# Optimization experiments

Hardware: AMD Instinct MI355X
Metric: run time of the kernel (lower is better)

Reference implementation:

```python
import jax, jax.numpy as jnp
import numpy as np

N_PARTIAL = 1024  # matches init_kwargs


def setup_inputs() -> dict:
    key = jax.random.key(0)
    k1, k2 = jax.random.split(key)
    B, H, L = 8, 768, 4096
    x = jax.random.normal(k1, (B, H, L), dtype=jnp.float32)
    k = jax.random.normal(k2, (H, L), dtype=jnp.float32)
    return {"x": x, "k": k}


def reference(x, k):
    # FFT-based causal long convolution with low-pass frequency truncation.
    L = x.shape[-1]
    N = 2 * L  # zero-pad to 2L for linear (non-circular) convolution
    x_dtype = x.dtype
    x_f = jnp.fft.rfft(x.astype(jnp.float32), n=N)          # [B, H, N//2+1] complex64
    k_f = jnp.fft.rfft(k.astype(jnp.float32), n=N)          # [H, N//2+1]   complex64
    # zero out all frequency bins >= N_partial // 2 (low-pass truncation of the kernel)
    freqs = jnp.arange(N // 2 + 1)
    k_f = jnp.where(freqs < N_PARTIAL // 2, k_f, jnp.zeros((), dtype=k_f.dtype))
    y_f = x_f * k_f                                          # broadcast over batch
    y = jnp.fft.irfft(y_f, n=N)[..., :L].astype(x_dtype)     # [B, H, L]
    return y
```

## Files before the change

kernel.cpp:

```cpp
#include <hip/hip_runtime.h>
#include <math.h>

#define LSEQ 4096
#define NFFT 8192
#define NF   512
#define NF2  1024
#define NH   768
#define NBH  6144
#define MROWS 6912

typedef __attribute__((ext_vector_type(8))) short short8;
typedef __attribute__((ext_vector_type(4))) float floatx4;

__device__ __forceinline__ unsigned short f2bf(float f) {
    unsigned int u = __float_as_uint(f);
    u += 0x7fff + ((u >> 16) & 1);
    return (unsigned short)(u >> 16);
}

__global__ void build_T1(unsigned short* __restrict__ T1) {
    int idx = blockIdx.x * blockDim.x + threadIdx.x;
    int f2 = idx >> 12;
    int n = idx & (LSEQ - 1);
    int f = f2 >> 1;
    int p = (f * n) & (NFFT - 1);
    float th = (float)p * (float)(2.0 * M_PI / (double)NFFT);
    float s, c;
    sincosf(th, &s, &c);
    T1[idx] = f2bf((f2 & 1) ? s : c);
}

__global__ void build_T2(unsigned short* __restrict__ T2) {
    int idx = blockIdx.x * blockDim.x + threadIdx.x;
    int n = idx >> 10;
    int f2 = idx & (NF2 - 1);
    int f = f2 >> 1;
    int p = (f * n) & (NFFT - 1);
    float th = (float)p * (float)(2.0 * M_PI / (double)NFFT);
    float s, c;
    sincosf(th, &s, &c);
    T2[idx] = f2bf((f2 & 1) ? s : c);
}

__global__ void tobf16(const float* __restrict__ x, const float* __restrict__ kk,
                       unsigned short* __restrict__ o) {
    size_t e = ((size_t)blockIdx.x * 256 + threadIdx.x) * 4;
    const size_t XN = (size_t)NBH * LSEQ;
    const float* s = (e < XN) ? (x + e) : (kk + (e - XN));
    float4 v = *(const float4*)s;
    unsigned int lo = (unsigned int)f2bf(v.x) | ((unsigned int)f2bf(v.y) << 16);
    unsigned int hi = (unsigned int)f2bf(v.z) | ((unsigned int)f2bf(v.w) << 16);
    *(uint2*)(o + e) = make_uint2(lo, hi);
}

__global__ __launch_bounds__(256) void gemm_bt(
    const unsigned short* __restrict__ A,
    const unsigned short* __restrict__ B,
    float* __restrict__ C,
    int M, int N, int K)
{
    __shared__ __align__(16) unsigned short As[128 * 32];
    __shared__ __align__(16) unsigned short Bs[128 * 32];
    const int t = threadIdx.x;
    const int w = t >> 6, l = t & 63;
    const int m0 = blockIdx.y * 128, n0 = blockIdx.x * 128;
    const int wm = (w >> 1) * 64, wn = (w & 1) * 64;
    const int lq = l >> 4;
    const int lr = l & 15;

    floatx4 acc[4][4];
#pragma unroll
    for (int i = 0; i < 4; ++i)
#pragma unroll
        for (int j = 0; j < 4; ++j)
            acc[i][j] = (floatx4){0.f, 0.f, 0.f, 0.f};

    const int q0 = t, q1 = t + 256;
    const int r0 = q0 >> 2, e0 = (q0 & 3) * 8;
    const int r1 = q1 >> 2, e1 = (q1 & 3) * 8;

    for (int k0 = 0; k0 < K; k0 += 32) {
        const unsigned short* ga0 = A + (size_t)(m0 + r0) * K + k0 + e0;
        const unsigned short* ga1 = A + (size_t)(m0 + r1) * K + k0 + e1;
        const unsigned short* gb0 = B + (size_t)(n0 + r0) * K + k0 + e0;
        const unsigned short* gb1 = B + (size_t)(n0 + r1) * K + k0 + e1;
        __builtin_amdgcn_global_load_lds((const __attribute__((address_space(1))) void*)ga0,
            (__attribute__((address_space(3))) void*)(As + q0 * 8), 16, 0, 0);
        __builtin_amdgcn_global_load_lds((const __attribute__((address_space(1))) void*)ga1,
            (__attribute__((address_space(3))) void*)(As + q1 * 8), 16, 0, 0);
        __builtin_amdgcn_global_load_lds((const __attribute__((address_space(1))) void*)gb0,
            (__attribute__((address_space(3))) void*)(Bs + q0 * 8), 16, 0, 0);
        __builtin_amdgcn_global_load_lds((const __attribute__((address_space(1))) void*)gb1,
            (__attribute__((address_space(3))) void*)(Bs + q1 * 8), 16, 0, 0);
        __syncthreads();

        short8 af[4], bfv[4];
#pragma unroll
        for (int i = 0; i < 4; ++i)
            af[i] = *(const short8*)(As + (wm + 16 * i + lr) * 32 + lq * 8);
#pragma unroll
        for (int j = 0; j < 4; ++j)
            bfv[j] = *(const short8*)(Bs + (wn + 16 * j + lr) * 32 + lq * 8);
#pragma unroll
        for (int i = 0; i < 4; ++i)
#pragma unroll
            for (int j = 0; j < 4; ++j)
                acc[i][j] = __builtin_amdgcn_mfma_f32_16x16x32_bf16(af[i], bfv[j], acc[i][j], 0, 0, 0);
        __syncthreads();
    }

#pragma unroll
    for (int i = 0; i < 4; ++i)
#pragma unroll
        for (int j = 0; j < 4; ++j)
#pragma unroll
            for (int r = 0; r < 4; ++r) {
                int row = m0 + wm + 16 * i + lq * 4 + r;
                int col = n0 + wn + 16 * j + lr;
                C[(size_t)row * N + col] = acc[i][j][r];
            }
}

__global__ void combine(const float* __restrict__ C1, unsigned short* __restrict__ AB) {
    int idx = blockIdx.x * blockDim.x + threadIdx.x;
    int bh = idx >> 9;
    int f = idx & (NF - 1);
    int h = bh % NH;
    const float* xc = C1 + (size_t)bh * NF2 + 2 * f;
    const float* kc = C1 + (size_t)(NBH + h) * NF2 + 2 * f;
    float Xre = xc[0], Xim = -xc[1];
    float Kre = kc[0], Kim = -kc[1];
    float s = (f == 0 ? 1.0f : 2.0f) * (1.0f / (float)NFFT);
    float Av = s * (Xre * Kre - Xim * Kim);
    float Bv = -(s * (Xre * Kim + Xim * Kre));
    AB[(size_t)bh * NF2 + 2 * f]     = f2bf(Av);
    AB[(size_t)bh * NF2 + 2 * f + 1] = f2bf(Bv);
}

extern "C" void kernel_launch(void* const* d_in, const int* in_sizes, int n_in,
                              void* d_out, int out_size, void* d_ws, size_t ws_size,
                              hipStream_t stream) {
    const float* x = (const float*)d_in[0];
    const float* k = (const float*)d_in[1];
    float* y = (float*)d_out;

    unsigned short* T1 = (unsigned short*)d_ws;
    unsigned short* T2 = T1 + (size_t)NF2 * LSEQ;
    unsigned short* AB = T2 + (size_t)LSEQ * NF2;

    unsigned short* Abm = (unsigned short*)d_out;
    float* C1 = (float*)((char*)d_out + (size_t)MROWS * LSEQ * 2);

    const int blk = 256;
    hipLaunchKernelGGL(build_T1, dim3((NF2 * LSEQ) / blk), dim3(blk), 0, stream, T1);
    hipLaunchKernelGGL(build_T2, dim3((LSEQ * NF2) / blk), dim3(blk), 0, stream, T2);
    hipLaunchKernelGGL(tobf16, dim3((MROWS * LSEQ / 4) / blk), dim3(blk), 0, stream, x, k, Abm);
    hipLaunchKernelGGL(gemm_bt, dim3(NF2 / 128, MROWS / 128), dim3(blk), 0, stream,
                       Abm, T1, C1, MROWS, NF2, LSEQ);
    hipLaunchKernelGGL(combine, dim3((NBH * NF) / blk), dim3(blk), 0, stream, C1, AB);
    hipLaunchKernelGGL(gemm_bt, dim3(LSEQ / 128, NBH / 128), dim3(blk), 0, stream,
                       AB, T2, y, NBH, LSEQ, NF2);
}
```

Measured before the change: 366.5 us.

## Split-K the forward DFT GEMM, fuse twiddle table builds, pack combine I/O

The first GEMM (6912x1024, K=4096) goes from 432 blocks to 864 by splitting K in two. Each half writes bf16 partials that the combine kernel sums, so the grid fills more of the GPU and the intermediate is half the bytes. The two twiddle-table kernels become one that computes each sincos once and writes the transposed copy through an LDS tile, and combine now uses packed 32-bit loads and stores. The cost is extra precision loss from rounding the partials to bf16 before they are summed, plus a second partial buffer to read.

```diff
diff --git a/kernel.cpp b/kernel.cpp
--- a/kernel.cpp
+++ b/kernel.cpp
@@ -8,6 +8,7 @@
 #define NH   768
 #define NBH  6144
 #define MROWS 6912
+#define KSPLIT 2
 
 typedef __attribute__((ext_vector_type(8))) short short8;
 typedef __attribute__((ext_vector_type(4))) float floatx4;
@@ -17,29 +18,37 @@
     u += 0x7fff + ((u >> 16) & 1);
     return (unsigned short)(u >> 16);
 }
-
-__global__ void build_T1(unsigned short* __restrict__ T1) {
-    int idx = blockIdx.x * blockDim.x + threadIdx.x;
-    int f2 = idx >> 12;
-    int n = idx & (LSEQ - 1);
-    int f = f2 >> 1;
-    int p = (f * n) & (NFFT - 1);
-    float th = (float)p * (float)(2.0 * M_PI / (double)NFFT);
-    float s, c;
-    sincosf(th, &s, &c);
-    T1[idx] = f2bf((f2 & 1) ? s : c);
-}
-
-__global__ void build_T2(unsigned short* __restrict__ T2) {
-    int idx = blockIdx.x * blockDim.x + threadIdx.x;
-    int n = idx >> 10;
-    int f2 = idx & (NF2 - 1);
-    int f = f2 >> 1;
-    int p = (f * n) & (NFFT - 1);
-    float th = (float)p * (float)(2.0 * M_PI / (double)NFFT);
-    float s, c;
-    sincosf(th, &s, &c);
-    T2[idx] = f2bf((f2 & 1) ? s : c);
+__device__ __forceinline__ float bf2f(unsigned int u16) {
+    return __uint_as_float(u16 << 16);
+}
+
+__global__ void build_tables(unsigned short* __restrict__ T1,
+                             unsigned short* __restrict__ T2) {
+    __shared__ unsigned short tile[64][66];
+    const int t = threadIdx.x;
+    const int F0 = blockIdx.x * 64;
+    const int N0 = blockIdx.y * 64;
+#pragma unroll
+    for (int i = 0; i < 16; ++i) {
+        int r = (t >> 6) + i * 4;
+        int c = t & 63;
+        int f2 = F0 + r, n = N0 + c;
+        int f = f2 >> 1;
+        int p = (f * n) & (NFFT - 1);
+        float th = (float)p * (float)(2.0 * M_PI / (double)NFFT);
+        float s, cc;
+        sincosf(th, &s, &cc);
+        unsigned short v = f2bf((f2 & 1) ? s : cc);
+        T1[(size_t)f2 * LSEQ + n] = v;
+        tile[r][c] = v;
+    }
+    __syncthreads();
+#pragma unroll
+    for (int i = 0; i < 16; ++i) {
+        int r = (t >> 6) + i * 4;
+        int c = t & 63;
+        T2[(size_t)(N0 + r) * NF2 + F0 + c] = tile[c][r];
+    }
 }
 
 __global__ void tobf16(const float* __restrict__ x, const float* __restrict__ kk,
@@ -51,6 +60,76 @@
     unsigned int lo = (unsigned int)f2bf(v.x) | ((unsigned int)f2bf(v.y) << 16);
     unsigned int hi = (unsigned int)f2bf(v.z) | ((unsigned int)f2bf(v.w) << 16);
     *(uint2*)(o + e) = make_uint2(lo, hi);
+}
+
+__global__ __launch_bounds__(256) void gemm_a_splitk(
+    const unsigned short* __restrict__ A,
+    const unsigned short* __restrict__ B,
+    unsigned short* __restrict__ P,
+    int M, int N, int K)
+{
+    __shared__ __align__(16) unsigned short As[128 * 32];
+    __shared__ __align__(16) unsigned short Bs[128 * 32];
+    const int t = threadIdx.x;
+    const int w = t >> 6, l = t & 63;
+    const int m0 = blockIdx.y * 128, n0 = blockIdx.x * 128;
+    const int wm = (w >> 1) * 64, wn = (w & 1) * 64;
+    const int lq = l >> 4, lr = l & 15;
+    const int kbeg = blockIdx.z * (K / KSPLIT);
+    const int kend = kbeg + K / KSPLIT;
+
+    floatx4 acc[4][4];
+#pragma unroll
+    for (int i = 0; i < 4; ++i)
+#pragma unroll
+        for (int j = 0; j < 4; ++j)
+            acc[i][j] = (floatx4){0.f, 0.f, 0.f, 0.f};
+
+    const int q0 = t, q1 = t + 256;
+    const int r0 = q0 >> 2, e0 = (q0 & 3) * 8;
+    const int r1 = q1 >> 2, e1 = (q1 & 3) * 8;
+
+    for (int k0 = kbeg; k0 < kend; k0 += 32) {
+        const unsigned short* ga0 = A + (size_t)(m0 + r0) * K + k0 + e0;
+        const unsigned short* ga1 = A + (size_t)(m0 + r1) * K + k0 + e1;
+        const unsigned short* gb0 = B + (size_t)(n0 + r0) * K + k0 + e0;
+        const unsigned short* gb1 = B + (size_t)(n0 + r1) * K + k0 + e1;
+        __builtin_amdgcn_global_load_lds((const __attribute__((address_space(1))) void*)ga0,
+            (__attribute__((address_space(3))) void*)(As + q0 * 8), 16, 0, 0);
+        __builtin_amdgcn_global_load_lds((const __attribute__((address_space(1))) void*)ga1,
+            (__attribute__((address_space(3))) void*)(As + q1 * 8), 16, 0, 0);
+        __builtin_amdgcn_global_load_lds((const __attribute__((address_space(1))) void*)gb0,
+            (__attribute__((address_space(3))) void*)(Bs + q0 * 8), 16, 0, 0);
+        __builtin_amdgcn_global_load_lds((const __attribute__((address_space(1))) void*)gb1,
+            (__attribute__((address_space(3))) void*)(Bs + q1 * 8), 16, 0, 0);
+        __syncthreads();
+
+        short8 af[4], bfv[4];
+#pragma unroll
+        for (int i = 0; i < 4; ++i)
+            af[i] = *(const short8*)(As + (wm + 16 * i + lr) * 32 + lq * 8);
+#pragma unroll
+        for (int j = 0; j < 4; ++j)
+            bfv[j] = *(const short8*)(Bs + (wn + 16 * j + lr) * 32 + lq * 8);
+#pragma unroll
+        for (int i = 0; i < 4; ++i)
+#pragma unroll
+            for (int j = 0; j < 4; ++j)
+                acc[i][j] = __builtin_amdgcn_mfma_f32_16x16x32_bf16(af[i], bfv[j], acc[i][j], 0, 0, 0);
+        __syncthreads();
+    }
+
+    unsigned short* Pz = P + (size_t)blockIdx.z * M * N;
+#pragma unroll
+    for (int i = 0; i < 4; ++i)
+#pragma unroll
+        for (int j = 0; j < 4; ++j)
+#pragma unroll
+            for (int r = 0; r < 4; ++r) {
+                int row = m0 + wm + 16 * i + lq * 4 + r;
+                int col = n0 + wn + 16 * j + lr;
+                Pz[(size_t)row * N + col] = f2bf(acc[i][j][r]);
+            }
 }
 
 __global__ __launch_bounds__(256) void gemm_bt(
@@ -65,8 +144,7 @@
     const int w = t >> 6, l = t & 63;
     const int m0 = blockIdx.y * 128, n0 = blockIdx.x * 128;
     const int wm = (w >> 1) * 64, wn = (w & 1) * 64;
-    const int lq = l >> 4;
-    const int lr = l & 15;
+    const int lq = l >> 4, lr = l & 15;
 
     floatx4 acc[4][4];
 #pragma unroll
@@ -121,20 +199,26 @@
             }
 }
 
-__global__ void combine(const float* __restrict__ C1, unsigned short* __restrict__ AB) {
+__global__ void combine(const unsigned short* __restrict__ P,
+                        unsigned short* __restrict__ AB) {
     int idx = blockIdx.x * blockDim.x + threadIdx.x;
     int bh = idx >> 9;
     int f = idx & (NF - 1);
     int h = bh % NH;
-    const float* xc = C1 + (size_t)bh * NF2 + 2 * f;
-    const float* kc = C1 + (size_t)(NBH + h) * NF2 + 2 * f;
-    float Xre = xc[0], Xim = -xc[1];
-    float Kre = kc[0], Kim = -kc[1];
+    const size_t PS = (size_t)MROWS * NF2;
+    unsigned int x0 = *(const unsigned int*)(P + (size_t)bh * NF2 + 2 * f);
+    unsigned int x1 = *(const unsigned int*)(P + PS + (size_t)bh * NF2 + 2 * f);
+    unsigned int k0 = *(const unsigned int*)(P + (size_t)(NBH + h) * NF2 + 2 * f);
+    unsigned int k1 = *(const unsigned int*)(P + PS + (size_t)(NBH + h) * NF2 + 2 * f);
+    float Xre = bf2f(x0 & 0xffff) + bf2f(x1 & 0xffff);
+    float Xim = -(bf2f(x0 >> 16) + bf2f(x1 >> 16));
+    float Kre = bf2f(k0 & 0xffff) + bf2f(k1 & 0xffff);
+    float Kim = -(bf2f(k0 >> 16) + bf2f(k1 >> 16));
     float s = (f == 0 ? 1.0f : 2.0f) * (1.0f / (float)NFFT);
     float Av = s * (Xre * Kre - Xim * Kim);
     float Bv = -(s * (Xre * Kim + Xim * Kre));
-    AB[(size_t)bh * NF2 + 2 * f]     = f2bf(Av);
-    AB[(size_t)bh * NF2 + 2 * f + 1] = f2bf(Bv);
+    unsigned int packed = (unsigned int)f2bf(Av) | ((unsigned int)f2bf(Bv) << 16);
+    *(unsigned int*)(AB + (size_t)bh * NF2 + 2 * f) = packed;
 }
 
 extern "C" void kernel_launch(void* const* d_in, const int* in_sizes, int n_in,
@@ -149,15 +233,14 @@
     unsigned short* AB = T2 + (size_t)LSEQ * NF2;
 
     unsigned short* Abm = (unsigned short*)d_out;
-    float* C1 = (float*)((char*)d_out + (size_t)MROWS * LSEQ * 2);
+    unsigned short* P = Abm + (size_t)MROWS * LSEQ;
 
     const int blk = 256;
-    hipLaunchKernelGGL(build_T1, dim3((NF2 * LSEQ) / blk), dim3(blk), 0, stream, T1);
-    hipLaunchKernelGGL(build_T2, dim3((LSEQ * NF2) / blk), dim3(blk), 0, stream, T2);
+    hipLaunchKernelGGL(build_tables, dim3(NF2 / 64, LSEQ / 64), dim3(blk), 0, stream, T1, T2);
     hipLaunchKernelGGL(tobf16, dim3((MROWS * LSEQ / 4) / blk), dim3(blk), 0, stream, x, k, Abm);
-    hipLaunchKernelGGL(gemm_bt, dim3(NF2 / 128, MROWS / 128), dim3(blk), 0, stream,
-                       Abm, T1, C1, MROWS, NF2, LSEQ);
-    hipLaunchKernelGGL(combine, dim3((NBH * NF) / blk), dim3(blk), 0, stream, C1, AB);
+    hipLaunchKernelGGL(gemm_a_splitk, dim3(NF2 / 128, MROWS / 128, KSPLIT), dim3(blk), 0, stream,
+                       Abm, T1, P, MROWS, NF2, LSEQ);
+    hipLaunchKernelGGL(combine, dim3((NBH * NF) / blk), dim3(blk), 0, stream, P, AB);
     hipLaunchKernelGGL(gemm_bt, dim3(LSEQ / 128, NBH / 128), dim3(blk), 0, stream,
                        AB, T2, y, NBH, LSEQ, NF2);
 }
```

Result: no change. 366.2 us (-0.1%).

## Double-buffer GEMM LDS tiles with register prefetch and fuse DFT table builds

Applied to the files above, without the earlier changes.

The GEMM main loop now uses two LDS buffers: the next K-tile is loaded into registers while MFMAs run on the current tile, then written to the other buffer, leaving one barrier per iteration instead of two. This replaces the direct global-to-LDS loads. The two DFT twiddle-table kernels are merged into one tiled kernel that computes each value once and writes the transpose through shared memory, and combine now stores each bf16 pair as a single 32-bit write. The trade-off is more registers and LDS per block, and the loss of the async global_load_lds path, which could lower occupancy.

```diff
diff --git a/kernel.cpp b/kernel.cpp
--- a/kernel.cpp
+++ b/kernel.cpp
@@ -18,28 +18,33 @@
     return (unsigned short)(u >> 16);
 }
 
-__global__ void build_T1(unsigned short* __restrict__ T1) {
-    int idx = blockIdx.x * blockDim.x + threadIdx.x;
-    int f2 = idx >> 12;
-    int n = idx & (LSEQ - 1);
-    int f = f2 >> 1;
-    int p = (f * n) & (NFFT - 1);
-    float th = (float)p * (float)(2.0 * M_PI / (double)NFFT);
-    float s, c;
-    sincosf(th, &s, &c);
-    T1[idx] = f2bf((f2 & 1) ? s : c);
-}
-
-__global__ void build_T2(unsigned short* __restrict__ T2) {
-    int idx = blockIdx.x * blockDim.x + threadIdx.x;
-    int n = idx >> 10;
-    int f2 = idx & (NF2 - 1);
-    int f = f2 >> 1;
-    int p = (f * n) & (NFFT - 1);
-    float th = (float)p * (float)(2.0 * M_PI / (double)NFFT);
-    float s, c;
-    sincosf(th, &s, &c);
-    T2[idx] = f2bf((f2 & 1) ? s : c);
+__global__ void build_tables(unsigned short* __restrict__ T1,
+                             unsigned short* __restrict__ T2) {
+    __shared__ unsigned short tile[64][66];
+    const int t = threadIdx.x;
+    const int F0 = blockIdx.x * 64;
+    const int N0 = blockIdx.y * 64;
+#pragma unroll
+    for (int i = 0; i < 16; ++i) {
+        int r = (t >> 6) + i * 4;
+        int c = t & 63;
+        int f2 = F0 + r, n = N0 + c;
+        int f = f2 >> 1;
+        int p = (f * n) & (NFFT - 1);
+        float th = (float)p * (float)(2.0 * M_PI / (double)NFFT);
+        float s, cc;
+        sincosf(th, &s, &cc);
+        unsigned short v = f2bf((f2 & 1) ? s : cc);
+        T1[(size_t)f2 * LSEQ + n] = v;
+        tile[r][c] = v;
+    }
+    __syncthreads();
+#pragma unroll
+    for (int i = 0; i < 16; ++i) {
+        int r = (t >> 6) + i * 4;
+        int c = t & 63;
+        T2[(size_t)(N0 + r) * NF2 + F0 + c] = tile[c][r];
+    }
 }
 
 __global__ void tobf16(const float* __restrict__ x, const float* __restrict__ kk,
@@ -59,14 +64,13 @@
     float* __restrict__ C,
     int M, int N, int K)
 {
-    __shared__ __align__(16) unsigned short As[128 * 32];
-    __shared__ __align__(16) unsigned short Bs[128 * 32];
+    __shared__ __align__(16) unsigned short As[2][128 * 32];
+    __shared__ __align__(16) unsigned short Bs[2][128 * 32];
     const int t = threadIdx.x;
     const int w = t >> 6, l = t & 63;
     const int m0 = blockIdx.y * 128, n0 = blockIdx.x * 128;
     const int wm = (w >> 1) * 64, wn = (w & 1) * 64;
-    const int lq = l >> 4;
-    const int lr = l & 15;
+    const int lq = l >> 4, lr = l & 15;
 
     floatx4 acc[4][4];
 #pragma unroll
@@ -78,35 +82,63 @@
     const int q0 = t, q1 = t + 256;
     const int r0 = q0 >> 2, e0 = (q0 & 3) * 8;
     const int r1 = q1 >> 2, e1 = (q1 & 3) * 8;
+    const unsigned short* pa0 = A + (size_t)(m0 + r0) * K + e0;
+    const unsigned short* pa1 = A + (size_t)(m0 + r1) * K + e1;
+    const unsigned short* pb0 = B + (size_t)(n0 + r0) * K + e0;
+    const unsigned short* pb1 = B + (size_t)(n0 + r1) * K + e1;
 
-    for (int k0 = 0; k0 < K; k0 += 32) {
-        const unsigned short* ga0 = A + (size_t)(m0 + r0) * K + k0 + e0;
-        const unsigned short* ga1 = A + (size_t)(m0 + r1) * K + k0 + e1;
-        const unsigned short* gb0 = B + (size_t)(n0 + r0) * K + k0 + e0;
-        const unsigned short* gb1 = B + (size_t)(n0 + r1) * K + k0 + e1;
-        __builtin_amdgcn_global_load_lds((const __attribute__((address_space(1))) void*)ga0,
-            (__attribute__((address_space(3))) void*)(As + q0 * 8), 16, 0, 0);
-        __builtin_amdgcn_global_load_lds((const __attribute__((address_space(1))) void*)ga1,
-            (__attribute__((address_space(3))) void*)(As + q1 * 8), 16, 0, 0);
-        __builtin_amdgcn_global_load_lds((const __attribute__((address_space(1))) void*)gb0,
-            (__attribute__((address_space(3))) void*)(Bs + q0 * 8), 16, 0, 0);
-        __builtin_amdgcn_global_load_lds((const __attribute__((address_space(1))) void*)gb1,
-            (__attribute__((address_space(3))) void*)(Bs + q1 * 8), 16, 0, 0);
-        __syncthreads();
+    uint4 ra0 = *(const uint4*)pa0;
+    uint4 ra1 = *(const uint4*)pa1;
+    uint4 rb0 = *(const uint4*)pb0;
+    uint4 rb1 = *(const uint4*)pb1;
+    *(uint4*)(As[0] + q0 * 8) = ra0;
+    *(uint4*)(As[0] + q1 * 8) = ra1;
+    *(uint4*)(Bs[0] + q0 * 8) = rb0;
+    *(uint4*)(Bs[0] + q1 * 8) = rb1;
+    __syncthreads();
+
+    int cur = 0;
+    for (int k0 = 32; k0 < K; k0 += 32) {
+        ra0 = *(const uint4*)(pa0 + k0);
+        ra1 = *(const uint4*)(pa1 + k0);
+        rb0 = *(const uint4*)(pb0 + k0);
+        rb1 = *(const uint4*)(pb1 + k0);
 
         short8 af[4], bfv[4];
 #pragma unroll
         for (int i = 0; i < 4; ++i)
-            af[i] = *(const short8*)(As + (wm + 16 * i + lr) * 32 + lq * 8);
+            af[i] = *(const short8*)(As[cur] + (wm + 16 * i + lr) * 32 + lq * 8);
 #pragma unroll
         for (int j = 0; j < 4; ++j)
-            bfv[j] = *(const short8*)(Bs + (wn + 16 * j + lr) * 32 + lq * 8);
+            bfv[j] = *(const short8*)(Bs[cur] + (wn + 16 * j + lr) * 32 + lq * 8);
 #pragma unroll
         for (int i = 0; i < 4; ++i)
 #pragma unroll
             for (int j = 0; j < 4; ++j)
                 acc[i][j] = __builtin_amdgcn_mfma_f32_16x16x32_bf16(af[i], bfv[j], acc[i][j], 0, 0, 0);
+
+        const int nxt = cur ^ 1;
+        *(uint4*)(As[nxt] + q0 * 8) = ra0;
+        *(uint4*)(As[nxt] + q1 * 8) = ra1;
+        *(uint4*)(Bs[nxt] + q0 * 8) = rb0;
+        *(uint4*)(Bs[nxt] + q1 * 8) = rb1;
         __syncthreads();
+        cur = nxt;
+    }
+
+    {
+        short8 af[4], bfv[4];
+#pragma unroll
+        for (int i = 0; i < 4; ++i)
+            af[i] = *(const short8*)(As[cur] + (wm + 16 * i + lr) * 32 + lq * 8);
+#pragma unroll
+        for (int j = 0; j < 4; ++j)
+            bfv[j] = *(const short8*)(Bs[cur] + (wn + 16 * j + lr) * 32 + lq * 8);
+#pragma unroll
+        for (int i = 0; i < 4; ++i)
+#pragma unroll
+            for (int j = 0; j < 4; ++j)
+                acc[i][j] = __builtin_amdgcn_mfma_f32_16x16x32_bf16(af[i], bfv[j], acc[i][j], 0, 0, 0);
     }
 
 #pragma unroll
@@ -133,8 +165,8 @@
     float s = (f == 0 ? 1.0f : 2.0f) * (1.0f / (float)NFFT);
     float Av = s * (Xre * Kre - Xim * Kim);
     float Bv = -(s * (Xre * Kim + Xim * Kre));
-    AB[(size_t)bh * NF2 + 2 * f]     = f2bf(Av);
-    AB[(size_t)bh * NF2 + 2 * f + 1] = f2bf(Bv);
+    unsigned int packed = (unsigned int)f2bf(Av) | ((unsigned int)f2bf(Bv) << 16);
+    *(unsigned int*)(AB + (size_t)bh * NF2 + 2 * f) = packed;
 }
 
 extern "C" void kernel_launch(void* const* d_in, const int* in_sizes, int n_in,
@@ -152,8 +184,7 @@
     float* C1 = (float*)((char*)d_out + (size_t)MROWS * LSEQ * 2);
 
     const int blk = 256;
-    hipLaunchKernelGGL(build_T1, dim3((NF2 * LSEQ) / blk), dim3(blk), 0, stream, T1);
-    hipLaunchKernelGGL(build_T2, dim3((LSEQ * NF2) / blk), dim3(blk), 0, stream, T2);
+    hipLaunchKernelGGL(build_tables, dim3(NF2 / 64, LSEQ / 64), dim3(blk), 0, stream, T1, T2);
     hipLaunchKernelGGL(tobf16, dim3((MROWS * LSEQ / 4) / blk), dim3(blk), 0, stream, x, k, Abm);
     hipLaunchKernelGGL(gemm_bt, dim3(NF2 / 128, MROWS / 128), dim3(blk), 0, stream,
                        Abm, T1, C1, MROWS, NF2, LSEQ);
```

Result: faster. 339.7 us (-7.3%).
